# Performance work log

Measured on AMD Instinct MI355X. Metric: run time of the kernel, lower is better.

The kernel has to match this reference:

```python
import math
import jax, jax.numpy as jnp
import numpy as np

B, S, G, CMAX, T = 128, 256, 8, 6, 32
E, NH, L, Z = 64, 4, 2, 3
DFF = 4 * E


def _conv1d(x, w, b, pad):
    # x: [N, C, T], w: [O, I, K] -> [N, O, T]
    y = jax.lax.conv_general_dilated(x, w, (1,), [(pad, pad)], dimension_numbers=('NCH', 'OIH', 'NCH'))
    return y + b[None, :, None]


def _layernorm(x, g, b, eps=1e-5):
    m = jnp.mean(x, -1, keepdims=True)
    v = jnp.mean((x - m) ** 2, -1, keepdims=True)
    return (x - m) * jax.lax.rsqrt(v + eps) * g + b


def _pos_encoding(seq_len, dim):
    pos = jnp.arange(seq_len, dtype=jnp.float32)[:, None]
    div = jnp.exp(jnp.arange(0, dim, 2, dtype=jnp.float32) * (-math.log(10000.0) / dim))
    pe = jnp.zeros((seq_len, dim), dtype=jnp.float32)
    pe = pe.at[:, 0::2].set(jnp.sin(pos * div)).at[:, 1::2].set(jnp.cos(pos * div))
    return pe


def setup_inputs() -> dict:
    key = jax.random.key(0)
    ks = iter(jax.random.split(key, 48))
    def nrm(shape, s=0.05):
        return (jax.random.normal(next(ks), shape) * s).astype(jnp.float32)
    inp = {}
    inp['waveforms'] = jax.random.normal(next(ks), (B, S, CMAX, T), dtype=jnp.float32)
    inp['shank_ids'] = jax.random.randint(next(ks), (B, S), 0, G)
    lengths = jax.random.randint(next(ks), (B,), S // 2, S + 1)
    inp['mask'] = jnp.arange(S)[None, :] >= lengths[:, None]  # True = padded
    inp['conv1_w'] = nrm((G, 32, CMAX, 5), 0.1)
    inp['conv1_b'] = jnp.zeros((G, 32), jnp.float32)
    inp['conv2_w'] = nrm((G, E, 32, 3), 0.1)
    inp['conv2_b'] = jnp.zeros((G, E), jnp.float32)
    inp['shank_emb'] = nrm((G, E), 0.02)
    inp['in_proj_w'] = nrm((L, 3 * E, E))
    inp['in_proj_b'] = jnp.zeros((L, 3 * E), jnp.float32)
    inp['out_proj_w'] = nrm((L, E, E))
    inp['out_proj_b'] = jnp.zeros((L, E), jnp.float32)
    inp['ln1_g'] = jnp.ones((L, E), jnp.float32)
    inp['ln1_b'] = jnp.zeros((L, E), jnp.float32)
    inp['ff1_w'] = nrm((L, DFF, E))
    inp['ff1_b'] = jnp.zeros((L, DFF), jnp.float32)
    inp['ff2_w'] = nrm((L, E, DFF))
    inp['ff2_b'] = jnp.zeros((L, E), jnp.float32)
    inp['ln2_g'] = jnp.ones((L, E), jnp.float32)
    inp['ln2_b'] = jnp.zeros((L, E), jnp.float32)
    inp['cls_w1'] = nrm((E, E)); inp['cls_b1'] = jnp.zeros((E,), jnp.float32)
    inp['cls_w2'] = nrm((Z, E)); inp['cls_b2'] = jnp.zeros((Z,), jnp.float32)
    inp['mu_w1'] = nrm((Z, E, E)); inp['mu_b1'] = jnp.zeros((Z, E), jnp.float32)
    inp['mu_w2'] = nrm((Z, 2, E)); inp['mu_b2'] = jnp.zeros((Z, 2), jnp.float32)
    inp['ls_w1'] = nrm((Z, E, E)); inp['ls_b1'] = jnp.zeros((Z, E), jnp.float32)
    inp['ls_w2'] = nrm((Z, 2, E)); inp['ls_b2'] = jnp.zeros((Z, 2), jnp.float32)
    inp['d_w1'] = nrm((E, E)); inp['d_b1'] = jnp.zeros((E,), jnp.float32)
    inp['d_w2'] = nrm((1, E)); inp['d_b2'] = jnp.zeros((1,), jnp.float32)
    return inp


def reference(waveforms, shank_ids, mask, conv1_w, conv1_b, conv2_w, conv2_b, shank_emb,
              in_proj_w, in_proj_b, out_proj_w, out_proj_b, ln1_g, ln1_b,
              ff1_w, ff1_b, ff2_w, ff2_b, ln2_g, ln2_b,
              cls_w1, cls_b1, cls_w2, cls_b2, mu_w1, mu_b1, mu_w2, mu_b2,
              ls_w1, ls_b1, ls_w2, ls_b2, d_w1, d_b1, d_w2, d_b2):
    b, s, c, t = waveforms.shape
    e = shank_emb.shape[1]
    g = shank_emb.shape[0]
    x = waveforms.reshape(b * s, c, t)
    # per-shank conv encoders (MoE-style dispatch); loop over fixed small expert set
    embs = []
    for i in range(g):
        h1 = jax.nn.relu(_conv1d(x, conv1_w[i], conv1_b[i], 2))   # [N,32,T]
        h2 = jax.nn.relu(_conv1d(h1, conv2_w[i], conv2_b[i], 1))  # [N,E,T]
        embs.append(h2.mean(-1))                                  # AdaptiveAvgPool1d(1)
    emb_all = jnp.stack(embs, axis=1)                             # [N,G,E]
    sid = shank_ids.reshape(-1)
    emb = jnp.take_along_axis(emb_all, sid[:, None, None], axis=1)[:, 0]  # [N,E]
    active = (~mask).reshape(-1)
    emb = jnp.where(active[:, None], emb, 0.0).reshape(b, s, e)   # masked slots stay zero
    emb = emb + shank_emb[shank_ids] + _pos_encoding(s, e)[None]
    # post-norm transformer encoder, relu FFN, eval mode (dropout off)
    dh = e // NH
    key_bias = jnp.where(mask, -1e9, 0.0).astype(emb.dtype)[:, None, None, :]  # [B,1,1,S]
    h = emb
    for l in range(in_proj_w.shape[0]):
        qkv = h @ in_proj_w[l].T + in_proj_b[l]
        q, k, v = jnp.split(qkv, 3, axis=-1)
        q = q.reshape(b, s, NH, dh)
        k = k.reshape(b, s, NH, dh)
        v = v.reshape(b, s, NH, dh)
        scores = jnp.einsum('bqhd,bkhd->bhqk', q, k) / math.sqrt(dh) + key_bias
        attn = jax.nn.softmax(scores, axis=-1)
        o = jnp.einsum('bhqk,bkhd->bqhd', attn, v).reshape(b, s, e)
        o = o @ out_proj_w[l].T + out_proj_b[l]
        h = _layernorm(h + o, ln1_g[l], ln1_b[l])
        ff = jax.nn.relu(h @ ff1_w[l].T + ff1_b[l]) @ ff2_w[l].T + ff2_b[l]
        h = _layernorm(h + ff, ln2_g[l], ln2_b[l])
    am = active.reshape(b, s, 1).astype(h.dtype)
    pooled = (h * am).sum(1) / (am.sum(1) + 1e-8)                 # masked mean pool [B,E]
    cls_logits = jax.nn.relu(pooled @ cls_w1.T + cls_b1) @ cls_w2.T + cls_b2
    hz = jax.nn.relu(jnp.einsum('be,zfe->zbf', pooled, mu_w1) + mu_b1[:, None])
    mus = jnp.einsum('zbf,zof->bzo', hz, mu_w2) + mu_b2[None]     # [B,Z,2]
    hs = jax.nn.relu(jnp.einsum('be,zfe->zbf', pooled, ls_w1) + ls_b1[:, None])
    sigmas = jnp.exp(jnp.einsum('zbf,zof->bzo', hs, ls_w2) + ls_b2[None])  # [B,Z,2]
    d_pred = jax.nn.sigmoid(jax.nn.relu(pooled @ d_w1.T + d_b1) @ d_w2.T + d_b2)
    return jnp.concatenate([cls_logits, mus.reshape(b, -1), sigmas.reshape(b, -1), d_pred], axis=-1)
```

## Files before the change

kernel.cpp:

```cpp
#include <hip/hip_runtime.h>
#include <math.h>


typedef short bf16x8 __attribute__((ext_vector_type(8)));
typedef float f32x4 __attribute__((ext_vector_type(4)));

__device__ __forceinline__ unsigned short f2bf(float f) {
  unsigned u = __float_as_uint(f);
  u += 0x7fffu + ((u >> 16) & 1u);
  return (unsigned short)(u >> 16);
}

__device__ __forceinline__ float bf2f(unsigned short s) {
  return __uint_as_float(((unsigned)s) << 16);
}

__device__ __forceinline__ bf16x8 ldfrag(const unsigned short* p) {
  return *reinterpret_cast<const bf16x8*>(p);
}

__device__ __forceinline__ bool is_masked(const void* mask_, int flag, int idx) {
  return flag ? (((const unsigned char*)mask_)[idx] != 0)
              : (((const int*)mask_)[idx] != 0);
}

__global__ void detect_mask_kernel(const unsigned int* __restrict__ mw,
                                   int* __restrict__ flag, int* __restrict__ counts,
                                   int* __restrict__ lens) {
  __shared__ int sh;
  if (threadIdx.x == 0) sh = 0;
  __syncthreads();
  int bad = 0;
  for (int i = threadIdx.x; i < 8192; i += 256)
    if (mw[i] > 1u) bad = 1;
  if (bad) atomicOr(&sh, 1);
  if (threadIdx.x < 8) counts[threadIdx.x] = 0;
  if (threadIdx.x < 128) lens[threadIdx.x] = 0;
  __syncthreads();
  if (threadIdx.x == 0) *flag = sh;
}

__global__ __launch_bounds__(256) void bin_kernel(
    const int* __restrict__ sid, const void* __restrict__ mask_,
    const int* __restrict__ flagp, int* __restrict__ counts,
    int* __restrict__ lens, int* __restrict__ idxbuf) {
  __shared__ int lcnt[8];
  __shared__ int lbase[8];
  int b = blockIdx.x, tid = threadIdx.x;
  int n = b * 256 + tid;
  int flag = *flagp;
  bool act = !is_masked(mask_, flag, n);
  int g = act ? sid[n] : 0;
  if (tid < 8) lcnt[tid] = 0;
  __syncthreads();
  int pos = 0;
  if (act) pos = atomicAdd(&lcnt[g], 1);
  __syncthreads();
  if (tid < 8) lbase[tid] = atomicAdd(&counts[tid], lcnt[tid]);
  if (tid == 0)
    lens[b] = lcnt[0] + lcnt[1] + lcnt[2] + lcnt[3] +
              lcnt[4] + lcnt[5] + lcnt[6] + lcnt[7];
  __syncthreads();
  if (act) idxbuf[g * 32768 + lbase[g] + pos] = n;
}

__global__ __launch_bounds__(256) void init_emb_kernel(
    const int* __restrict__ sid, const float* __restrict__ shank_emb,
    float* __restrict__ hout) {
  int i = blockIdx.x * 256 + threadIdx.x;
  int n = i >> 6, e = i & 63, s = n & 255;
  int g = sid[n];
  float div = __expf(-(float)(e & ~1) * (9.21034037f / 64.f));
  float angle = (float)s * div;
  float pe = (e & 1) ? cosf(angle) : sinf(angle);
  hout[i] = shank_emb[g * 64 + e] + pe;
}

__global__ __launch_bounds__(256) void conv_mfma_kernel(
    const int* __restrict__ idxbuf, const int* __restrict__ counts,
    const float* __restrict__ wav,
    const float* __restrict__ w1_, const float* __restrict__ b1_,
    const float* __restrict__ w2_, const float* __restrict__ b2_,
    const float* __restrict__ shank_emb, float* __restrict__ hout) {
  __shared__ __align__(16) unsigned short w1f[5][32][8];
  __shared__ __align__(16) unsigned short w2f[3][64][40];
  __shared__ float b1s[32];
  __shared__ float b2s[64];
  __shared__ __align__(16) unsigned short xw[4][36][8];
  __shared__ __align__(16) unsigned short h1w[4][34][40];
  int g = blockIdx.x & 7, bib = blockIdx.x >> 3;
  int tid = threadIdx.x;
  int wv = tid >> 6, lane = tid & 63, quad = lane >> 4, l15 = lane & 15;
  for (int i = tid; i < 1280; i += 256) {
    int k = i >> 8, rest = i & 255, oc = rest >> 3, ic = rest & 7;
    w1f[k][oc][ic] = (ic < 6) ? f2bf(w1_[g * 960 + oc * 30 + ic * 5 + k]) : 0;
  }
  for (int i = tid; i < 7680; i += 256) {
    int k = i / 2560, rest = i % 2560, e = rest / 40, ic = rest % 40;
    w2f[k][e][ic] = (ic < 32) ? f2bf(w2_[g * 6144 + e * 96 + ic * 3 + k]) : 0;
  }
  if (tid < 32) b1s[tid] = b1_[g * 32 + tid];
  if (tid < 64) b2s[tid] = b2_[g * 64 + tid];
  {
    unsigned int* xz = (unsigned int*)&xw[wv][0][0];
    for (int i = lane; i < 144; i += 64) xz[i] = 0;
    unsigned int* hz0 = (unsigned int*)&h1w[wv][0][0];
    unsigned int* hz1 = (unsigned int*)&h1w[wv][33][0];
    if (lane < 20) hz0[lane] = 0;
    else if (lane < 40) hz1[lane - 20] = 0;
  }
  __syncthreads();
  bf16x8 zf = {0, 0, 0, 0, 0, 0, 0, 0};
  bf16x8 bf1[2], bf1k4[2], bf2[3][4];
#pragma unroll
  for (int nt = 0; nt < 2; nt++) {
    bf1[nt] = ldfrag(&w1f[quad][nt * 16 + l15][0]);
    bf1k4[nt] = (quad == 0) ? ldfrag(&w1f[4][nt * 16 + l15][0]) : zf;
  }
#pragma unroll
  for (int k = 0; k < 3; k++)
#pragma unroll
    for (int nt = 0; nt < 4; nt++)
      bf2[k][nt] = ldfrag(&w2f[k][nt * 16 + l15][quad * 8]);
  float b1v0 = b1s[l15], b1v1 = b1s[16 + l15];
  float shank = shank_emb[g * 64 + lane];
  float dive = __expf(-(float)(lane & ~1) * (9.21034037f / 64.f));
  int cnt = counts[g];
  int wvg = bib * 4 + wv;
  int ic_w = lane >> 3, t0_w = (lane & 7) * 4;
  for (int ti = wvg; ti < cnt; ti += 512) {
    int n = idxbuf[g * 32768 + ti];
    float4 v = make_float4(0.f, 0.f, 0.f, 0.f);
    if (lane < 48) v = *(const float4*)&wav[n * 192 + lane * 4];
    if (lane < 48) {
      xw[wv][t0_w + 2][ic_w] = f2bf(v.x);
      xw[wv][t0_w + 3][ic_w] = f2bf(v.y);
      xw[wv][t0_w + 4][ic_w] = f2bf(v.z);
      xw[wv][t0_w + 5][ic_w] = f2bf(v.w);
    }
    f32x4 c1[2][2];
#pragma unroll
    for (int mt = 0; mt < 2; mt++) {
      c1[mt][0] = (f32x4){b1v0, b1v0, b1v0, b1v0};
      c1[mt][1] = (f32x4){b1v1, b1v1, b1v1, b1v1};
    }
#pragma unroll
    for (int mt = 0; mt < 2; mt++) {
      bf16x8 afm = ldfrag(&xw[wv][mt * 16 + l15 + quad][0]);
      bf16x8 af4 = (quad == 0) ? ldfrag(&xw[wv][mt * 16 + l15 + 4][0]) : zf;
#pragma unroll
      for (int nt = 0; nt < 2; nt++) {
        c1[mt][nt] = __builtin_amdgcn_mfma_f32_16x16x32_bf16(afm, bf1[nt], c1[mt][nt], 0, 0, 0);
        c1[mt][nt] = __builtin_amdgcn_mfma_f32_16x16x32_bf16(af4, bf1k4[nt], c1[mt][nt], 0, 0, 0);
      }
    }
#pragma unroll
    for (int mt = 0; mt < 2; mt++)
#pragma unroll
      for (int nt = 0; nt < 2; nt++)
#pragma unroll
        for (int r = 0; r < 4; r++) {
          int t = mt * 16 + quad * 4 + r;
          h1w[wv][t + 1][nt * 16 + l15] = f2bf(fmaxf(c1[mt][nt][r], 0.f));
        }
    f32x4 c2[2][4];
#pragma unroll
    for (int mt = 0; mt < 2; mt++)
#pragma unroll
      for (int nt = 0; nt < 4; nt++) {
        float bv = b2s[nt * 16 + l15];
        c2[mt][nt] = (f32x4){bv, bv, bv, bv};
      }
#pragma unroll
    for (int k = 0; k < 3; k++)
#pragma unroll
      for (int mt = 0; mt < 2; mt++) {
        bf16x8 af = ldfrag(&h1w[wv][mt * 16 + l15 + k][quad * 8]);
#pragma unroll
        for (int nt = 0; nt < 4; nt++)
          c2[mt][nt] = __builtin_amdgcn_mfma_f32_16x16x32_bf16(af, bf2[k][nt], c2[mt][nt], 0, 0, 0);
      }
    float sums[4];
#pragma unroll
    for (int nt = 0; nt < 4; nt++) {
      float s = 0.f;
#pragma unroll
      for (int mt = 0; mt < 2; mt++)
#pragma unroll
        for (int r = 0; r < 4; r++) s += fmaxf(c2[mt][nt][r], 0.f);
      s += __shfl_xor(s, 16);
      s += __shfl_xor(s, 32);
      sums[nt] = s;
    }
    float t0 = __shfl(sums[0], l15);
    float t1 = __shfl(sums[1], l15);
    float t2 = __shfl(sums[2], l15);
    float t3 = __shfl(sums[3], l15);
    float val = (quad == 0) ? t0 : (quad == 1) ? t1 : (quad == 2) ? t2 : t3;
    float angle = (float)(n & 255) * dive;
    float pe = (lane & 1) ? cosf(angle) : sinf(angle);
    hout[(size_t)n * 64 + lane] = val * (1.f / 32.f) + shank + pe;
  }
}

__global__ __launch_bounds__(256) void gemm_qkv(
    const float* __restrict__ A, const float* __restrict__ W,
    const float* __restrict__ bias, float* __restrict__ C) {
  __shared__ __align__(16) unsigned short As[64][72];
  __shared__ __align__(16) unsigned short Bs[192][72];
  int m0 = blockIdx.x * 64;
  int tid = threadIdx.x;
  int wv = tid >> 6, lane = tid & 63, quad = lane >> 4, l15 = lane & 15;
  f32x4 acc[12];
#pragma unroll
  for (int nt = 0; nt < 12; nt++) {
    float b = bias[nt * 16 + l15];
    acc[nt] = (f32x4){b, b, b, b};
  }
  for (int i = tid; i < 1024; i += 256) {
    int r = i >> 4, c4 = (i & 15) << 2;
    float4 av = *(const float4*)&A[(size_t)(m0 + r) * 64 + c4];
    short4 t;
    t.x = (short)f2bf(av.x); t.y = (short)f2bf(av.y);
    t.z = (short)f2bf(av.z); t.w = (short)f2bf(av.w);
    *(short4*)&As[r][c4] = t;
  }
  for (int i = tid; i < 3072; i += 256) {
    int r = i >> 4, c4 = (i & 15) << 2;
    float4 wv4 = *(const float4*)&W[(size_t)r * 64 + c4];
    short4 u;
    u.x = (short)f2bf(wv4.x); u.y = (short)f2bf(wv4.y);
    u.z = (short)f2bf(wv4.z); u.w = (short)f2bf(wv4.w);
    *(short4*)&Bs[r][c4] = u;
  }
  __syncthreads();
#pragma unroll
  for (int ks = 0; ks < 64; ks += 32) {
    bf16x8 af = ldfrag(&As[wv * 16 + l15][ks + quad * 8]);
#pragma unroll
    for (int nt = 0; nt < 12; nt++) {
      bf16x8 bfr = ldfrag(&Bs[nt * 16 + l15][ks + quad * 8]);
      acc[nt] = __builtin_amdgcn_mfma_f32_16x16x32_bf16(af, bfr, acc[nt], 0, 0, 0);
    }
  }
  int mrow = m0 + wv * 16 + quad * 4;
#pragma unroll
  for (int nt = 0; nt < 12; nt++)
#pragma unroll
    for (int r = 0; r < 4; r++)
      C[(size_t)(mrow + r) * 192 + nt * 16 + l15] = acc[nt][r];
}

__global__ __launch_bounds__(256) void fused_rl_kernel(
    const float* __restrict__ obuf, float* __restrict__ H,
    const float* __restrict__ Wout, const float* __restrict__ bout,
    const float* __restrict__ ln1g, const float* __restrict__ ln1b,
    const float* __restrict__ Wff1, const float* __restrict__ bff1,
    const float* __restrict__ Wff2, const float* __restrict__ bff2,
    const float* __restrict__ ln2g, const float* __restrict__ ln2b) {
  __shared__ __align__(16) unsigned short Ao[64][72];
  __shared__ __align__(16) unsigned short Wo[64][72];
  __shared__ __align__(16) unsigned short W1s[256][72];
  __shared__ __align__(16) unsigned short W2s[64][264];
  __shared__ __align__(16) unsigned short h1b[64][72];
  __shared__ __align__(16) unsigned short ffa[64][264];
  __shared__ float h1f[64][68];
  int m0 = blockIdx.x * 64;
  int tid = threadIdx.x;
  int wv = tid >> 6, lane = tid & 63, quad = lane >> 4, l15 = lane & 15;
  for (int i = tid; i < 1024; i += 256) {
    int r = i >> 4, c4 = (i & 15) << 2;
    float4 av = *(const float4*)&obuf[(size_t)(m0 + r) * 64 + c4];
    short4 t;
    t.x = (short)f2bf(av.x); t.y = (short)f2bf(av.y);
    t.z = (short)f2bf(av.z); t.w = (short)f2bf(av.w);
    *(short4*)&Ao[r][c4] = t;
    float4 wv4 = *(const float4*)&Wout[(size_t)r * 64 + c4];
    short4 u;
    u.x = (short)f2bf(wv4.x); u.y = (short)f2bf(wv4.y);
    u.z = (short)f2bf(wv4.z); u.w = (short)f2bf(wv4.w);
    *(short4*)&Wo[r][c4] = u;
  }
  for (int i = tid; i < 4096; i += 256) {
    int r = i >> 4, c4 = (i & 15) << 2;
    float4 wv4 = *(const float4*)&Wff1[(size_t)r * 64 + c4];
    short4 u;
    u.x = (short)f2bf(wv4.x); u.y = (short)f2bf(wv4.y);
    u.z = (short)f2bf(wv4.z); u.w = (short)f2bf(wv4.w);
    *(short4*)&W1s[r][c4] = u;
  }
  for (int i = tid; i < 4096; i += 256) {
    int r = i >> 6, c4 = (i & 63) << 2;
    float4 wv4 = *(const float4*)&Wff2[(size_t)r * 256 + c4];
    short4 u;
    u.x = (short)f2bf(wv4.x); u.y = (short)f2bf(wv4.y);
    u.z = (short)f2bf(wv4.z); u.w = (short)f2bf(wv4.w);
    *(short4*)&W2s[r][c4] = u;
  }
  __syncthreads();
  int lr = wv * 16 + quad * 4;
  f32x4 acc[4];
#pragma unroll
  for (int nt = 0; nt < 4; nt++) {
    float b = bout[nt * 16 + l15];
    acc[nt] = (f32x4){b, b, b, b};
  }
#pragma unroll
  for (int ks = 0; ks < 64; ks += 32) {
    bf16x8 af = ldfrag(&Ao[wv * 16 + l15][ks + quad * 8]);
#pragma unroll
    for (int nt = 0; nt < 4; nt++) {
      bf16x8 bfr = ldfrag(&Wo[nt * 16 + l15][ks + quad * 8]);
      acc[nt] = __builtin_amdgcn_mfma_f32_16x16x32_bf16(af, bfr, acc[nt], 0, 0, 0);
    }
  }
#pragma unroll
  for (int r = 0; r < 4; r++) {
    float rv[4];
    float s = 0.f;
#pragma unroll
    for (int nt = 0; nt < 4; nt++) {
      float v = acc[nt][r] + H[(size_t)(m0 + lr + r) * 64 + nt * 16 + l15];
      rv[nt] = v; s += v;
    }
    s += __shfl_xor(s, 1); s += __shfl_xor(s, 2);
    s += __shfl_xor(s, 4); s += __shfl_xor(s, 8);
    float mean = s * (1.f / 64.f);
    float vsum = 0.f;
#pragma unroll
    for (int nt = 0; nt < 4; nt++) { rv[nt] -= mean; vsum += rv[nt] * rv[nt]; }
    vsum += __shfl_xor(vsum, 1); vsum += __shfl_xor(vsum, 2);
    vsum += __shfl_xor(vsum, 4); vsum += __shfl_xor(vsum, 8);
    float inv = rsqrtf(vsum * (1.f / 64.f) + 1e-5f);
#pragma unroll
    for (int nt = 0; nt < 4; nt++) {
      int col = nt * 16 + l15;
      float hv = rv[nt] * inv * ln1g[col] + ln1b[col];
      h1f[lr + r][col] = hv;
      h1b[lr + r][col] = f2bf(hv);
    }
  }
  f32x4 a2[16];
#pragma unroll
  for (int nt = 0; nt < 16; nt++) {
    float b = bff1[nt * 16 + l15];
    a2[nt] = (f32x4){b, b, b, b};
  }
#pragma unroll
  for (int ks = 0; ks < 64; ks += 32) {
    bf16x8 af = ldfrag(&h1b[wv * 16 + l15][ks + quad * 8]);
#pragma unroll
    for (int nt = 0; nt < 16; nt++) {
      bf16x8 bfr = ldfrag(&W1s[nt * 16 + l15][ks + quad * 8]);
      a2[nt] = __builtin_amdgcn_mfma_f32_16x16x32_bf16(af, bfr, a2[nt], 0, 0, 0);
    }
  }
#pragma unroll
  for (int nt = 0; nt < 16; nt++)
#pragma unroll
    for (int r = 0; r < 4; r++)
      ffa[lr + r][nt * 16 + l15] = f2bf(fmaxf(a2[nt][r], 0.f));
#pragma unroll
  for (int nt = 0; nt < 4; nt++) {
    float b = bff2[nt * 16 + l15];
    acc[nt] = (f32x4){b, b, b, b};
  }
#pragma unroll
  for (int ks = 0; ks < 256; ks += 32) {
    bf16x8 af = ldfrag(&ffa[wv * 16 + l15][ks + quad * 8]);
#pragma unroll
    for (int nt = 0; nt < 4; nt++) {
      bf16x8 bfr = ldfrag(&W2s[nt * 16 + l15][ks + quad * 8]);
      acc[nt] = __builtin_amdgcn_mfma_f32_16x16x32_bf16(af, bfr, acc[nt], 0, 0, 0);
    }
  }
#pragma unroll
  for (int r = 0; r < 4; r++) {
    float rv[4];
    float s = 0.f;
#pragma unroll
    for (int nt = 0; nt < 4; nt++) {
      float v = acc[nt][r] + h1f[lr + r][nt * 16 + l15];
      rv[nt] = v; s += v;
    }
    s += __shfl_xor(s, 1); s += __shfl_xor(s, 2);
    s += __shfl_xor(s, 4); s += __shfl_xor(s, 8);
    float mean = s * (1.f / 64.f);
    float vsum = 0.f;
#pragma unroll
    for (int nt = 0; nt < 4; nt++) { rv[nt] -= mean; vsum += rv[nt] * rv[nt]; }
    vsum += __shfl_xor(vsum, 1); vsum += __shfl_xor(vsum, 2);
    vsum += __shfl_xor(vsum, 4); vsum += __shfl_xor(vsum, 8);
    float inv = rsqrtf(vsum * (1.f / 64.f) + 1e-5f);
#pragma unroll
    for (int nt = 0; nt < 4; nt++) {
      int col = nt * 16 + l15;
      H[(size_t)(m0 + lr + r) * 64 + col] = rv[nt] * inv * ln2g[col] + ln2b[col];
    }
  }
}

__global__ __launch_bounds__(256) void attn_kernel(
    const float* __restrict__ qkv, const int* __restrict__ lens,
    float* __restrict__ o) {
  __shared__ __align__(16) unsigned short qs[256][24];
  __shared__ __align__(16) unsigned short kst[256][24];
  __shared__ __align__(16) unsigned short vT[16][264];
  __shared__ __align__(16) unsigned short pw[4][16][264];
  int bh = blockIdx.x;
  int b_ = bh >> 2, hd = bh & 3;
  int tid = threadIdx.x;
  int wv = tid >> 6, lane = tid & 63, quad = lane >> 4, l15 = lane & 15;
  int len = lens[b_];
  const float* base = qkv + b_ * 256 * 192 + hd * 16;
  for (int i = tid; i < 1024; i += 256) {
    int s = i >> 2, c = (i & 3) << 2;
    const float* rp = base + s * 192;
    float4 q4 = *(const float4*)(rp + c);
    float4 k4 = *(const float4*)(rp + 64 + c);
    float4 v4 = *(const float4*)(rp + 128 + c);
    short4 qp, kp;
    qp.x = (short)f2bf(q4.x * 0.25f); qp.y = (short)f2bf(q4.y * 0.25f);
    qp.z = (short)f2bf(q4.z * 0.25f); qp.w = (short)f2bf(q4.w * 0.25f);
    kp.x = (short)f2bf(k4.x); kp.y = (short)f2bf(k4.y);
    kp.z = (short)f2bf(k4.z); kp.w = (short)f2bf(k4.w);
    *(short4*)&qs[s][c] = qp;
    *(short4*)&kst[s][c] = kp;
    vT[c + 0][s] = f2bf(v4.x);
    vT[c + 1][s] = f2bf(v4.y);
    vT[c + 2][s] = f2bf(v4.z);
    vT[c + 3][s] = f2bf(v4.w);
  }
  __syncthreads();
  bf16x8 zf = {0, 0, 0, 0, 0, 0, 0, 0};
  f32x4 zero = {0.f, 0.f, 0.f, 0.f};
#pragma unroll 1
  for (int j = 0; j < 4; j++) {
    int qt = wv * 4 + j;
    bf16x8 bq = (quad < 2) ? ldfrag(&qs[qt * 16 + l15][quad * 8]) : zf;
    f32x4 s[16];
#pragma unroll
    for (int t = 0; t < 16; t++) {
      bf16x8 ak = (quad < 2) ? ldfrag(&kst[t * 16 + l15][quad * 8]) : zf;
      s[t] = __builtin_amdgcn_mfma_f32_16x16x32_bf16(ak, bq, zero, 0, 0, 0);
    }
    float mx = -1e30f;
#pragma unroll
    for (int t = 0; t < 16; t++)
#pragma unroll
      for (int r = 0; r < 4; r++) {
        int key = t * 16 + quad * 4 + r;
        float v = (key < len) ? s[t][r] : -1e30f;
        s[t][r] = v;
        mx = fmaxf(mx, v);
      }
    mx = fmaxf(mx, __shfl_xor(mx, 16));
    mx = fmaxf(mx, __shfl_xor(mx, 32));
    float sum = 0.f;
#pragma unroll
    for (int t = 0; t < 16; t++)
#pragma unroll
      for (int r = 0; r < 4; r++) {
        float p = __expf(s[t][r] - mx);
        s[t][r] = p;
        sum += p;
      }
    sum += __shfl_xor(sum, 16);
    sum += __shfl_xor(sum, 32);
#pragma unroll
    for (int t = 0; t < 16; t++) {
      short4 pp;
      pp.x = (short)f2bf(s[t][0]); pp.y = (short)f2bf(s[t][1]);
      pp.z = (short)f2bf(s[t][2]); pp.w = (short)f2bf(s[t][3]);
      *(short4*)&pw[wv][l15][t * 16 + quad * 4] = pp;
    }
    f32x4 acc = zero;
#pragma unroll
    for (int c = 0; c < 8; c++) {
      bf16x8 av = ldfrag(&vT[l15][c * 32 + quad * 8]);
      bf16x8 bp = ldfrag(&pw[wv][l15][c * 32 + quad * 8]);
      acc = __builtin_amdgcn_mfma_f32_16x16x32_bf16(av, bp, acc, 0, 0, 0);
    }
    float inv = 1.f / sum;
    float4 w;
    w.x = acc[0] * inv; w.y = acc[1] * inv;
    w.z = acc[2] * inv; w.w = acc[3] * inv;
    *(float4*)&o[(size_t)(b_ * 256 + qt * 16 + l15) * 64 + hd * 16 + quad * 4] = w;
  }
}

__global__ __launch_bounds__(256) void pool_kernel(
    const float* __restrict__ h, const int* __restrict__ lens,
    float* __restrict__ pooled) {
  __shared__ float ps[4][64];
  int b = blockIdx.x;
  int e = threadIdx.x & 63, sp = threadIdx.x >> 6;
  int len = lens[b];
  float sum = 0.f;
  int send = min(sp * 64 + 64, len);
  for (int s = sp * 64; s < send; s++) sum += h[(b * 256 + s) * 64 + e];
  ps[sp][e] = sum;
  __syncthreads();
  if (sp == 0) {
    float tot = ps[0][e] + ps[1][e] + ps[2][e] + ps[3][e];
    pooled[b * 64 + e] = tot / ((float)len + 1e-8f);
  }
}

__global__ __launch_bounds__(64) void heads_kernel(
    const float* __restrict__ pooled,
    const float* __restrict__ cls_w1, const float* __restrict__ cls_b1,
    const float* __restrict__ cls_w2, const float* __restrict__ cls_b2,
    const float* __restrict__ mu_w1, const float* __restrict__ mu_b1,
    const float* __restrict__ mu_w2, const float* __restrict__ mu_b2,
    const float* __restrict__ ls_w1, const float* __restrict__ ls_b1,
    const float* __restrict__ ls_w2, const float* __restrict__ ls_b2,
    const float* __restrict__ d_w1, const float* __restrict__ d_b1,
    const float* __restrict__ d_w2, const float* __restrict__ d_b2,
    float* __restrict__ out) {
  int b = blockIdx.x, e = threadIdx.x;
  __shared__ float p[64];
  __shared__ float t1[64];
  p[e] = pooled[b * 64 + e];
  __syncthreads();
  {
    float a = cls_b1[e];
    for (int j = 0; j < 64; j++) a += p[j] * cls_w1[e * 64 + j];
    t1[e] = fmaxf(a, 0.f);
  }
  __syncthreads();
  if (e < 3) {
    float a2 = cls_b2[e];
    for (int j = 0; j < 64; j++) a2 += t1[j] * cls_w2[e * 64 + j];
    out[b * 16 + e] = a2;
  }
  for (int z = 0; z < 3; z++) {
    __syncthreads();
    {
      float a = mu_b1[z * 64 + e];
      for (int j = 0; j < 64; j++) a += p[j] * mu_w1[(z * 64 + e) * 64 + j];
      t1[e] = fmaxf(a, 0.f);
    }
    __syncthreads();
    if (e < 2) {
      float a2 = mu_b2[z * 2 + e];
      for (int j = 0; j < 64; j++) a2 += t1[j] * mu_w2[(z * 2 + e) * 64 + j];
      out[b * 16 + 3 + z * 2 + e] = a2;
    }
    __syncthreads();
    {
      float a = ls_b1[z * 64 + e];
      for (int j = 0; j < 64; j++) a += p[j] * ls_w1[(z * 64 + e) * 64 + j];
      t1[e] = fmaxf(a, 0.f);
    }
    __syncthreads();
    if (e < 2) {
      float a2 = ls_b2[z * 2 + e];
      for (int j = 0; j < 64; j++) a2 += t1[j] * ls_w2[(z * 2 + e) * 64 + j];
      out[b * 16 + 9 + z * 2 + e] = __expf(a2);
    }
  }
  __syncthreads();
  {
    float a = d_b1[e];
    for (int j = 0; j < 64; j++) a += p[j] * d_w1[e * 64 + j];
    t1[e] = fmaxf(a, 0.f);
  }
  __syncthreads();
  if (e == 0) {
    float a2 = d_b2[0];
    for (int j = 0; j < 64; j++) a2 += t1[j] * d_w2[j];
    out[b * 16 + 15] = 1.f / (1.f + __expf(-a2));
  }
}

extern "C" void kernel_launch(void* const* d_in, const int* in_sizes, int n_in,
                              void* d_out, int out_size, void* d_ws, size_t ws_size,
                              hipStream_t stream) {
  const float* wav       = (const float*)d_in[0];
  const int*   sid       = (const int*)d_in[1];
  const void*  mask      = d_in[2];
  const float* conv1_w   = (const float*)d_in[3];
  const float* conv1_b   = (const float*)d_in[4];
  const float* conv2_w   = (const float*)d_in[5];
  const float* conv2_b   = (const float*)d_in[6];
  const float* shank_emb = (const float*)d_in[7];
  const float* in_proj_w = (const float*)d_in[8];
  const float* in_proj_b = (const float*)d_in[9];
  const float* out_proj_w= (const float*)d_in[10];
  const float* out_proj_b= (const float*)d_in[11];
  const float* ln1_g     = (const float*)d_in[12];
  const float* ln1_b     = (const float*)d_in[13];
  const float* ff1_w     = (const float*)d_in[14];
  const float* ff1_b     = (const float*)d_in[15];
  const float* ff2_w     = (const float*)d_in[16];
  const float* ff2_b     = (const float*)d_in[17];
  const float* ln2_g     = (const float*)d_in[18];
  const float* ln2_b     = (const float*)d_in[19];
  const float* cls_w1    = (const float*)d_in[20];
  const float* cls_b1    = (const float*)d_in[21];
  const float* cls_w2    = (const float*)d_in[22];
  const float* cls_b2    = (const float*)d_in[23];
  const float* mu_w1     = (const float*)d_in[24];
  const float* mu_b1     = (const float*)d_in[25];
  const float* mu_w2     = (const float*)d_in[26];
  const float* mu_b2     = (const float*)d_in[27];
  const float* ls_w1     = (const float*)d_in[28];
  const float* ls_b1     = (const float*)d_in[29];
  const float* ls_w2     = (const float*)d_in[30];
  const float* ls_b2     = (const float*)d_in[31];
  const float* d_w1      = (const float*)d_in[32];
  const float* d_b1      = (const float*)d_in[33];
  const float* d_w2      = (const float*)d_in[34];
  const float* d_b2      = (const float*)d_in[35];
  float* out = (float*)d_out;

  float* ws = (float*)d_ws;
  float* h      = ws;
  float* qkv    = ws + 2097152;
  float* obuf   = ws + 8388608;
  float* pooled = ws + 10485760;
  int*   ip     = (int*)(ws + 10493952);
  int*   flag   = ip;
  int*   counts = ip + 8;
  int*   lens   = ip + 16;
  int*   idxbuf = ip + 144;

  detect_mask_kernel<<<1, 256, 0, stream>>>((const unsigned int*)mask, flag, counts, lens);
  bin_kernel<<<128, 256, 0, stream>>>(sid, mask, flag, counts, lens, idxbuf);
  init_emb_kernel<<<8192, 256, 0, stream>>>(sid, shank_emb, h);
  conv_mfma_kernel<<<1024, 256, 0, stream>>>(idxbuf, counts, wav, conv1_w, conv1_b,
                                             conv2_w, conv2_b, shank_emb, h);
  for (int l = 0; l < 2; l++) {
    gemm_qkv<<<512, 256, 0, stream>>>(h, in_proj_w + l * 12288, in_proj_b + l * 192, qkv);
    attn_kernel<<<512, 256, 0, stream>>>(qkv, lens, obuf);
    fused_rl_kernel<<<512, 256, 0, stream>>>(
        obuf, h, out_proj_w + l * 4096, out_proj_b + l * 64,
        ln1_g + l * 64, ln1_b + l * 64,
        ff1_w + l * 16384, ff1_b + l * 256,
        ff2_w + l * 16384, ff2_b + l * 64,
        ln2_g + l * 64, ln2_b + l * 64);
  }
  pool_kernel<<<128, 256, 0, stream>>>(h, lens, pooled);
  heads_kernel<<<128, 64, 0, stream>>>(pooled, cls_w1, cls_b1, cls_w2, cls_b2,
                                       mu_w1, mu_b1, mu_w2, mu_b2,
                                       ls_w1, ls_b1, ls_w2, ls_b2,
                                       d_w1, d_b1, d_w2, d_b2, out);
}
```

Baseline: 340.8 us.

## Fuse QKV projection into attention kernel and merge pooling with heads

The separate QKV GEMM is removed. Each attention block (one per batch and head) now loads that sequence's hidden states and the 16-row Q/K/V weight slices, computes Q, K and V^T in shared memory with MFMA, and runs attention directly. This avoids writing and re-reading the full QKV tensor in global memory and saves one launch per layer, but the hidden states are reloaded four times, once per head. Pooling and the output heads are also merged into one kernel to drop a launch and the pooled buffer.

Result: faster. 321.9 us (-5.5%).

```diff
diff --git a/kernel.cpp b/kernel.cpp
--- a/kernel.cpp
+++ b/kernel.cpp
@@ -9,10 +9,6 @@
   unsigned u = __float_as_uint(f);
   u += 0x7fffu + ((u >> 16) & 1u);
   return (unsigned short)(u >> 16);
-}
-
-__device__ __forceinline__ float bf2f(unsigned short s) {
-  return __uint_as_float(((unsigned)s) << 16);
 }
 
 __device__ __forceinline__ bf16x8 ldfrag(const unsigned short* p) {
@@ -90,7 +86,7 @@
   __shared__ __align__(16) unsigned short h1w[4][34][40];
   int g = blockIdx.x & 7, bib = blockIdx.x >> 3;
   int tid = threadIdx.x;
-  int wv = tid >> 6, lane = tid & 63, quad = lane >> 4, l15 = lane & 15;
+  int wvx = tid >> 6, lane = tid & 63, quad = lane >> 4, l15 = lane & 15;
   for (int i = tid; i < 1280; i += 256) {
     int k = i >> 8, rest = i & 255, oc = rest >> 3, ic = rest & 7;
     w1f[k][oc][ic] = (ic < 6) ? f2bf(w1_[g * 960 + oc * 30 + ic * 5 + k]) : 0;
@@ -102,10 +98,10 @@
   if (tid < 32) b1s[tid] = b1_[g * 32 + tid];
   if (tid < 64) b2s[tid] = b2_[g * 64 + tid];
   {
-    unsigned int* xz = (unsigned int*)&xw[wv][0][0];
+    unsigned int* xz = (unsigned int*)&xw[wvx][0][0];
     for (int i = lane; i < 144; i += 64) xz[i] = 0;
-    unsigned int* hz0 = (unsigned int*)&h1w[wv][0][0];
-    unsigned int* hz1 = (unsigned int*)&h1w[wv][33][0];
+    unsigned int* hz0 = (unsigned int*)&h1w[wvx][0][0];
+    unsigned int* hz1 = (unsigned int*)&h1w[wvx][33][0];
     if (lane < 20) hz0[lane] = 0;
     else if (lane < 40) hz1[lane - 20] = 0;
   }
@@ -126,17 +122,17 @@
   float shank = shank_emb[g * 64 + lane];
   float dive = __expf(-(float)(lane & ~1) * (9.21034037f / 64.f));
   int cnt = counts[g];
-  int wvg = bib * 4 + wv;
+  int wvg = bib * 4 + wvx;
   int ic_w = lane >> 3, t0_w = (lane & 7) * 4;
   for (int ti = wvg; ti < cnt; ti += 512) {
     int n = idxbuf[g * 32768 + ti];
     float4 v = make_float4(0.f, 0.f, 0.f, 0.f);
     if (lane < 48) v = *(const float4*)&wav[n * 192 + lane * 4];
     if (lane < 48) {
-      xw[wv][t0_w + 2][ic_w] = f2bf(v.x);
-      xw[wv][t0_w + 3][ic_w] = f2bf(v.y);
-      xw[wv][t0_w + 4][ic_w] = f2bf(v.z);
-      xw[wv][t0_w + 5][ic_w] = f2bf(v.w);
+      xw[wvx][t0_w + 2][ic_w] = f2bf(v.x);
+      xw[wvx][t0_w + 3][ic_w] = f2bf(v.y);
+      xw[wvx][t0_w + 4][ic_w] = f2bf(v.z);
+      xw[wvx][t0_w + 5][ic_w] = f2bf(v.w);
     }
     f32x4 c1[2][2];
 #pragma unroll
@@ -146,8 +142,8 @@
     }
 #pragma unroll
     for (int mt = 0; mt < 2; mt++) {
-      bf16x8 afm = ldfrag(&xw[wv][mt * 16 + l15 + quad][0]);
-      bf16x8 af4 = (quad == 0) ? ldfrag(&xw[wv][mt * 16 + l15 + 4][0]) : zf;
+      bf16x8 afm = ldfrag(&xw[wvx][mt * 16 + l15 + quad][0]);
+      bf16x8 af4 = (quad == 0) ? ldfrag(&xw[wvx][mt * 16 + l15 + 4][0]) : zf;
 #pragma unroll
       for (int nt = 0; nt < 2; nt++) {
         c1[mt][nt] = __builtin_amdgcn_mfma_f32_16x16x32_bf16(afm, bf1[nt], c1[mt][nt], 0, 0, 0);
@@ -161,7 +157,7 @@
 #pragma unroll
         for (int r = 0; r < 4; r++) {
           int t = mt * 16 + quad * 4 + r;
-          h1w[wv][t + 1][nt * 16 + l15] = f2bf(fmaxf(c1[mt][nt][r], 0.f));
+          h1w[wvx][t + 1][nt * 16 + l15] = f2bf(fmaxf(c1[mt][nt][r], 0.f));
         }
     f32x4 c2[2][4];
 #pragma unroll
@@ -175,7 +171,7 @@
     for (int k = 0; k < 3; k++)
 #pragma unroll
       for (int mt = 0; mt < 2; mt++) {
-        bf16x8 af = ldfrag(&h1w[wv][mt * 16 + l15 + k][quad * 8]);
+        bf16x8 af = ldfrag(&h1w[wvx][mt * 16 + l15 + k][quad * 8]);
 #pragma unroll
         for (int nt = 0; nt < 4; nt++)
           c2[mt][nt] = __builtin_amdgcn_mfma_f32_16x16x32_bf16(af, bf2[k][nt], c2[mt][nt], 0, 0, 0);
@@ -203,52 +199,129 @@
   }
 }
 
-__global__ __launch_bounds__(256) void gemm_qkv(
-    const float* __restrict__ A, const float* __restrict__ W,
-    const float* __restrict__ bias, float* __restrict__ C) {
-  __shared__ __align__(16) unsigned short As[64][72];
-  __shared__ __align__(16) unsigned short Bs[192][72];
-  int m0 = blockIdx.x * 64;
+__global__ __launch_bounds__(256) void attn_fused_kernel(
+    const float* __restrict__ H, const float* __restrict__ Wqkv,
+    const float* __restrict__ bqkv, const int* __restrict__ lens,
+    float* __restrict__ o) {
+  __shared__ __align__(16) unsigned short un[18432];
+  __shared__ __align__(16) unsigned short wqs[16][72];
+  __shared__ __align__(16) unsigned short wks[16][72];
+  __shared__ __align__(16) unsigned short wvs[16][72];
+  __shared__ __align__(16) unsigned short qs[256][24];
+  __shared__ __align__(16) unsigned short kst[256][24];
+  __shared__ __align__(16) unsigned short vT[16][264];
+  __shared__ float bqs[16], bks[16], bvs[16];
+  unsigned short (*hs)[72] = (unsigned short(*)[72])un;
+  unsigned short (*pw)[16][264] = (unsigned short(*)[16][264])un;
+  int bh = blockIdx.x;
+  int b_ = bh >> 2, hd = bh & 3;
   int tid = threadIdx.x;
-  int wv = tid >> 6, lane = tid & 63, quad = lane >> 4, l15 = lane & 15;
-  f32x4 acc[12];
-#pragma unroll
-  for (int nt = 0; nt < 12; nt++) {
-    float b = bias[nt * 16 + l15];
-    acc[nt] = (f32x4){b, b, b, b};
-  }
-  for (int i = tid; i < 1024; i += 256) {
+  int wvx = tid >> 6, lane = tid & 63, quad = lane >> 4, l15 = lane & 15;
+  int len = lens[b_];
+  const float* hb = H + (size_t)b_ * 256 * 64;
+  for (int i = tid; i < 4096; i += 256) {
     int r = i >> 4, c4 = (i & 15) << 2;
-    float4 av = *(const float4*)&A[(size_t)(m0 + r) * 64 + c4];
+    float4 v = *(const float4*)&hb[r * 64 + c4];
     short4 t;
-    t.x = (short)f2bf(av.x); t.y = (short)f2bf(av.y);
-    t.z = (short)f2bf(av.z); t.w = (short)f2bf(av.w);
-    *(short4*)&As[r][c4] = t;
-  }
-  for (int i = tid; i < 3072; i += 256) {
+    t.x = (short)f2bf(v.x); t.y = (short)f2bf(v.y);
+    t.z = (short)f2bf(v.z); t.w = (short)f2bf(v.w);
+    *(short4*)&hs[r][c4] = t;
+  }
+  for (int i = tid; i < 768; i += 256) {
     int r = i >> 4, c4 = (i & 15) << 2;
-    float4 wv4 = *(const float4*)&W[(size_t)r * 64 + c4];
-    short4 u;
-    u.x = (short)f2bf(wv4.x); u.y = (short)f2bf(wv4.y);
-    u.z = (short)f2bf(wv4.z); u.w = (short)f2bf(wv4.w);
-    *(short4*)&Bs[r][c4] = u;
-  }
-  __syncthreads();
-#pragma unroll
-  for (int ks = 0; ks < 64; ks += 32) {
-    bf16x8 af = ldfrag(&As[wv * 16 + l15][ks + quad * 8]);
-#pragma unroll
-    for (int nt = 0; nt < 12; nt++) {
-      bf16x8 bfr = ldfrag(&Bs[nt * 16 + l15][ks + quad * 8]);
-      acc[nt] = __builtin_amdgcn_mfma_f32_16x16x32_bf16(af, bfr, acc[nt], 0, 0, 0);
-    }
-  }
-  int mrow = m0 + wv * 16 + quad * 4;
-#pragma unroll
-  for (int nt = 0; nt < 12; nt++)
-#pragma unroll
-    for (int r = 0; r < 4; r++)
-      C[(size_t)(mrow + r) * 192 + nt * 16 + l15] = acc[nt][r];
+    int which = r >> 4, rr = r & 15;
+    float4 v = *(const float4*)&Wqkv[(size_t)(which * 64 + hd * 16 + rr) * 64 + c4];
+    float sc = (which == 0) ? 0.25f : 1.f;
+    short4 t;
+    t.x = (short)f2bf(v.x * sc); t.y = (short)f2bf(v.y * sc);
+    t.z = (short)f2bf(v.z * sc); t.w = (short)f2bf(v.w * sc);
+    unsigned short (*dst)[72] = (which == 0) ? wqs : (which == 1) ? wks : wvs;
+    *(short4*)&dst[rr][c4] = t;
+  }
+  if (tid < 16) {
+    bqs[tid] = 0.25f * bqkv[hd * 16 + tid];
+    bks[tid] = bqkv[64 + hd * 16 + tid];
+    bvs[tid] = bqkv[128 + hd * 16 + tid];
+  }
+  __syncthreads();
+#pragma unroll
+  for (int t4 = 0; t4 < 4; t4++) {
+    int tile = wvx * 4 + t4;
+    float bq = bqs[l15], bk = bks[l15];
+    f32x4 aq = (f32x4){bq, bq, bq, bq};
+    f32x4 ak = (f32x4){bk, bk, bk, bk};
+    f32x4 av = (f32x4){bvs[quad * 4 + 0], bvs[quad * 4 + 1],
+                       bvs[quad * 4 + 2], bvs[quad * 4 + 3]};
+#pragma unroll
+    for (int ks = 0; ks < 64; ks += 32) {
+      bf16x8 af = ldfrag(&hs[tile * 16 + l15][ks + quad * 8]);
+      aq = __builtin_amdgcn_mfma_f32_16x16x32_bf16(af, ldfrag(&wqs[l15][ks + quad * 8]), aq, 0, 0, 0);
+      ak = __builtin_amdgcn_mfma_f32_16x16x32_bf16(af, ldfrag(&wks[l15][ks + quad * 8]), ak, 0, 0, 0);
+      av = __builtin_amdgcn_mfma_f32_16x16x32_bf16(ldfrag(&wvs[l15][ks + quad * 8]), af, av, 0, 0, 0);
+    }
+#pragma unroll
+    for (int r = 0; r < 4; r++) {
+      qs[tile * 16 + quad * 4 + r][l15] = f2bf(aq[r]);
+      kst[tile * 16 + quad * 4 + r][l15] = f2bf(ak[r]);
+      vT[quad * 4 + r][tile * 16 + l15] = f2bf(av[r]);
+    }
+  }
+  __syncthreads();
+  bf16x8 zf = {0, 0, 0, 0, 0, 0, 0, 0};
+  f32x4 zero = {0.f, 0.f, 0.f, 0.f};
+#pragma unroll 1
+  for (int j = 0; j < 4; j++) {
+    int qt = wvx * 4 + j;
+    bf16x8 bq = (quad < 2) ? ldfrag(&qs[qt * 16 + l15][quad * 8]) : zf;
+    f32x4 s[16];
+#pragma unroll
+    for (int t = 0; t < 16; t++) {
+      bf16x8 ak = (quad < 2) ? ldfrag(&kst[t * 16 + l15][quad * 8]) : zf;
+      s[t] = __builtin_amdgcn_mfma_f32_16x16x32_bf16(ak, bq, zero, 0, 0, 0);
+    }
+    float mx = -1e30f;
+#pragma unroll
+    for (int t = 0; t < 16; t++)
+#pragma unroll
+      for (int r = 0; r < 4; r++) {
+        int key = t * 16 + quad * 4 + r;
+        float v = (key < len) ? s[t][r] : -1e30f;
+        s[t][r] = v;
+        mx = fmaxf(mx, v);
+      }
+    mx = fmaxf(mx, __shfl_xor(mx, 16));
+    mx = fmaxf(mx, __shfl_xor(mx, 32));
+    float sum = 0.f;
+#pragma unroll
+    for (int t = 0; t < 16; t++)
+#pragma unroll
+      for (int r = 0; r < 4; r++) {
+        float p = __expf(s[t][r] - mx);
+        s[t][r] = p;
+        sum += p;
+      }
+    sum += __shfl_xor(sum, 16);
+    sum += __shfl_xor(sum, 32);
+#pragma unroll
+    for (int t = 0; t < 16; t++) {
+      short4 pp;
+      pp.x = (short)f2bf(s[t][0]); pp.y = (short)f2bf(s[t][1]);
+      pp.z = (short)f2bf(s[t][2]); pp.w = (short)f2bf(s[t][3]);
+      *(short4*)&pw[wvx][l15][t * 16 + quad * 4] = pp;
+    }
+    f32x4 acc = zero;
+#pragma unroll
+    for (int c = 0; c < 8; c++) {
+      bf16x8 avv = ldfrag(&vT[l15][c * 32 + quad * 8]);
+      bf16x8 bp = ldfrag(&pw[wvx][l15][c * 32 + quad * 8]);
+      acc = __builtin_amdgcn_mfma_f32_16x16x32_bf16(avv, bp, acc, 0, 0, 0);
+    }
+    float inv = 1.f / sum;
+    float4 w;
+    w.x = acc[0] * inv; w.y = acc[1] * inv;
+    w.z = acc[2] * inv; w.w = acc[3] * inv;
+    *(float4*)&o[(size_t)(b_ * 256 + qt * 16 + l15) * 64 + hd * 16 + quad * 4] = w;
+  }
 }
 
 __global__ __launch_bounds__(256) void fused_rl_kernel(
@@ -267,7 +340,7 @@
   __shared__ float h1f[64][68];
   int m0 = blockIdx.x * 64;
   int tid = threadIdx.x;
-  int wv = tid >> 6, lane = tid & 63, quad = lane >> 4, l15 = lane & 15;
+  int wvx = tid >> 6, lane = tid & 63, quad = lane >> 4, l15 = lane & 15;
   for (int i = tid; i < 1024; i += 256) {
     int r = i >> 4, c4 = (i & 15) << 2;
     float4 av = *(const float4*)&obuf[(size_t)(m0 + r) * 64 + c4];
@@ -298,7 +371,7 @@
     *(short4*)&W2s[r][c4] = u;
   }
   __syncthreads();
-  int lr = wv * 16 + quad * 4;
+  int lr = wvx * 16 + quad * 4;
   f32x4 acc[4];
 #pragma unroll
   for (int nt = 0; nt < 4; nt++) {
@@ -307,7 +380,7 @@
   }
 #pragma unroll
   for (int ks = 0; ks < 64; ks += 32) {
-    bf16x8 af = ldfrag(&Ao[wv * 16 + l15][ks + quad * 8]);
+    bf16x8 af = ldfrag(&Ao[wvx * 16 + l15][ks + quad * 8]);
 #pragma unroll
     for (int nt = 0; nt < 4; nt++) {
       bf16x8 bfr = ldfrag(&Wo[nt * 16 + l15][ks + quad * 8]);
@@ -348,7 +421,7 @@
   }
 #pragma unroll
   for (int ks = 0; ks < 64; ks += 32) {
-    bf16x8 af = ldfrag(&h1b[wv * 16 + l15][ks + quad * 8]);
+    bf16x8 af = ldfrag(&h1b[wvx * 16 + l15][ks + quad * 8]);
 #pragma unroll
     for (int nt = 0; nt < 16; nt++) {
       bf16x8 bfr = ldfrag(&W1s[nt * 16 + l15][ks + quad * 8]);
@@ -367,7 +440,7 @@
   }
 #pragma unroll
   for (int ks = 0; ks < 256; ks += 32) {
-    bf16x8 af = ldfrag(&ffa[wv * 16 + l15][ks + quad * 8]);
+    bf16x8 af = ldfrag(&ffa[wvx * 16 + l15][ks + quad * 8]);
 #pragma unroll
     for (int nt = 0; nt < 4; nt++) {
       bf16x8 bfr = ldfrag(&W2s[nt * 16 + l15][ks + quad * 8]);
@@ -400,115 +473,8 @@
   }
 }
 
-__global__ __launch_bounds__(256) void attn_kernel(
-    const float* __restrict__ qkv, const int* __restrict__ lens,
-    float* __restrict__ o) {
-  __shared__ __align__(16) unsigned short qs[256][24];
-  __shared__ __align__(16) unsigned short kst[256][24];
-  __shared__ __align__(16) unsigned short vT[16][264];
-  __shared__ __align__(16) unsigned short pw[4][16][264];
-  int bh = blockIdx.x;
-  int b_ = bh >> 2, hd = bh & 3;
-  int tid = threadIdx.x;
-  int wv = tid >> 6, lane = tid & 63, quad = lane >> 4, l15 = lane & 15;
-  int len = lens[b_];
-  const float* base = qkv + b_ * 256 * 192 + hd * 16;
-  for (int i = tid; i < 1024; i += 256) {
-    int s = i >> 2, c = (i & 3) << 2;
-    const float* rp = base + s * 192;
-    float4 q4 = *(const float4*)(rp + c);
-    float4 k4 = *(const float4*)(rp + 64 + c);
-    float4 v4 = *(const float4*)(rp + 128 + c);
-    short4 qp, kp;
-    qp.x = (short)f2bf(q4.x * 0.25f); qp.y = (short)f2bf(q4.y * 0.25f);
-    qp.z = (short)f2bf(q4.z * 0.25f); qp.w = (short)f2bf(q4.w * 0.25f);
-    kp.x = (short)f2bf(k4.x); kp.y = (short)f2bf(k4.y);
-    kp.z = (short)f2bf(k4.z); kp.w = (short)f2bf(k4.w);
-    *(short4*)&qs[s][c] = qp;
-    *(short4*)&kst[s][c] = kp;
-    vT[c + 0][s] = f2bf(v4.x);
-    vT[c + 1][s] = f2bf(v4.y);
-    vT[c + 2][s] = f2bf(v4.z);
-    vT[c + 3][s] = f2bf(v4.w);
-  }
-  __syncthreads();
-  bf16x8 zf = {0, 0, 0, 0, 0, 0, 0, 0};
-  f32x4 zero = {0.f, 0.f, 0.f, 0.f};
-#pragma unroll 1
-  for (int j = 0; j < 4; j++) {
-    int qt = wv * 4 + j;
-    bf16x8 bq = (quad < 2) ? ldfrag(&qs[qt * 16 + l15][quad * 8]) : zf;
-    f32x4 s[16];
-#pragma unroll
-    for (int t = 0; t < 16; t++) {
-      bf16x8 ak = (quad < 2) ? ldfrag(&kst[t * 16 + l15][quad * 8]) : zf;
-      s[t] = __builtin_amdgcn_mfma_f32_16x16x32_bf16(ak, bq, zero, 0, 0, 0);
-    }
-    float mx = -1e30f;
-#pragma unroll
-    for (int t = 0; t < 16; t++)
-#pragma unroll
-      for (int r = 0; r < 4; r++) {
-        int key = t * 16 + quad * 4 + r;
-        float v = (key < len) ? s[t][r] : -1e30f;
-        s[t][r] = v;
-        mx = fmaxf(mx, v);
-      }
-    mx = fmaxf(mx, __shfl_xor(mx, 16));
-    mx = fmaxf(mx, __shfl_xor(mx, 32));
-    float sum = 0.f;
-#pragma unroll
-    for (int t = 0; t < 16; t++)
-#pragma unroll
-      for (int r = 0; r < 4; r++) {
-        float p = __expf(s[t][r] - mx);
-        s[t][r] = p;
-        sum += p;
-      }
-    sum += __shfl_xor(sum, 16);
-    sum += __shfl_xor(sum, 32);
-#pragma unroll
-    for (int t = 0; t < 16; t++) {
-      short4 pp;
-      pp.x = (short)f2bf(s[t][0]); pp.y = (short)f2bf(s[t][1]);
-      pp.z = (short)f2bf(s[t][2]); pp.w = (short)f2bf(s[t][3]);
-      *(short4*)&pw[wv][l15][t * 16 + quad * 4] = pp;
-    }
-    f32x4 acc = zero;
-#pragma unroll
-    for (int c = 0; c < 8; c++) {
-      bf16x8 av = ldfrag(&vT[l15][c * 32 + quad * 8]);
-      bf16x8 bp = ldfrag(&pw[wv][l15][c * 32 + quad * 8]);
-      acc = __builtin_amdgcn_mfma_f32_16x16x32_bf16(av, bp, acc, 0, 0, 0);
-    }
-    float inv = 1.f / sum;
-    float4 w;
-    w.x = acc[0] * inv; w.y = acc[1] * inv;
-    w.z = acc[2] * inv; w.w = acc[3] * inv;
-    *(float4*)&o[(size_t)(b_ * 256 + qt * 16 + l15) * 64 + hd * 16 + quad * 4] = w;
-  }
-}
-
-__global__ __launch_bounds__(256) void pool_kernel(
+__global__ __launch_bounds__(256) void pool_heads_kernel(
     const float* __restrict__ h, const int* __restrict__ lens,
-    float* __restrict__ pooled) {
-  __shared__ float ps[4][64];
-  int b = blockIdx.x;
-  int e = threadIdx.x & 63, sp = threadIdx.x >> 6;
-  int len = lens[b];
-  float sum = 0.f;
-  int send = min(sp * 64 + 64, len);
-  for (int s = sp * 64; s < send; s++) sum += h[(b * 256 + s) * 64 + e];
-  ps[sp][e] = sum;
-  __syncthreads();
-  if (sp == 0) {
-    float tot = ps[0][e] + ps[1][e] + ps[2][e] + ps[3][e];
-    pooled[b * 64 + e] = tot / ((float)len + 1e-8f);
-  }
-}
-
-__global__ __launch_bounds__(64) void heads_kernel(
-    const float* __restrict__ pooled,
     const float* __restrict__ cls_w1, const float* __restrict__ cls_b1,
     const float* __restrict__ cls_w2, const float* __restrict__ cls_b2,
     const float* __restrict__ mu_w1, const float* __restrict__ mu_b1,
@@ -518,56 +484,67 @@
     const float* __restrict__ d_w1, const float* __restrict__ d_b1,
     const float* __restrict__ d_w2, const float* __restrict__ d_b2,
     float* __restrict__ out) {
-  int b = blockIdx.x, e = threadIdx.x;
+  __shared__ float ps[4][64];
   __shared__ float p[64];
   __shared__ float t1[64];
-  p[e] = pooled[b * 64 + e];
-  __syncthreads();
+  int b = blockIdx.x, tid = threadIdx.x;
+  int e = tid & 63, sp = tid >> 6;
+  int len = lens[b];
   {
-    float a = cls_b1[e];
-    for (int j = 0; j < 64; j++) a += p[j] * cls_w1[e * 64 + j];
-    t1[e] = fmaxf(a, 0.f);
-  }
-  __syncthreads();
-  if (e < 3) {
-    float a2 = cls_b2[e];
-    for (int j = 0; j < 64; j++) a2 += t1[j] * cls_w2[e * 64 + j];
-    out[b * 16 + e] = a2;
+    float sum = 0.f;
+    int send = min(sp * 64 + 64, len);
+    for (int s = sp * 64; s < send; s++) sum += h[(size_t)(b * 256 + s) * 64 + e];
+    ps[sp][e] = sum;
+  }
+  __syncthreads();
+  if (sp == 0)
+    p[e] = (ps[0][e] + ps[1][e] + ps[2][e] + ps[3][e]) / ((float)len + 1e-8f);
+  __syncthreads();
+  if (tid < 64) {
+    float a = cls_b1[tid];
+    for (int j = 0; j < 64; j++) a += p[j] * cls_w1[tid * 64 + j];
+    t1[tid] = fmaxf(a, 0.f);
+  }
+  __syncthreads();
+  if (tid < 3) {
+    float a2 = cls_b2[tid];
+    for (int j = 0; j < 64; j++) a2 += t1[j] * cls_w2[tid * 64 + j];
+    out[b * 16 + tid] = a2;
   }
   for (int z = 0; z < 3; z++) {
     __syncthreads();
-    {
-      float a = mu_b1[z * 64 + e];
-      for (int j = 0; j < 64; j++) a += p[j] * mu_w1[(z * 64 + e) * 64 + j];
-      t1[e] = fmaxf(a, 0.f);
+    if (tid < 64) {
+      float a = mu_b1[z * 64 + tid];
+      for (int j = 0; j < 64; j++) a += p[j] * mu_w1[(z * 64 + tid) * 64 + j];
+      t1[tid] = fmaxf(a, 0.f);
     }
     __syncthreads();
-    if (e < 2) {
-      float a2 = mu_b2[z * 2 + e];
-      for (int j = 0; j < 64; j++) a2 += t1[j] * mu_w2[(z * 2 + e) * 64 + j];
-      out[b * 16 + 3 + z * 2 + e] = a2;
+    if (tid < 2) {
+      float a2 = mu_b2[z * 2 + tid];
+      for (int j = 0; j < 64; j++) a2 += t1[j] * mu_w2[(z * 2 + tid) * 64 + j];
+      out[b * 16 + 3 + z * 2 + tid] = a2;
     }
     __syncthreads();
-    {
-      float a = ls_b1[z * 64 + e];
-      for (int j = 0; j < 64; j++) a += p[j] * ls_w1[(z * 64 + e) * 64 + j];
-      t1[e] = fmaxf(a, 0.f);
+    if (tid < 64) {
+      float a = ls_b1[z * 64 + tid];
+      for (int j = 0; j < 64; j++) a += p[j] * ls_w1[(z * 64 + tid) * 64 + j];
+      t1[tid] = fmaxf(a, 0.f);
     }
     __syncthreads();
-    if (e < 2) {
-      float a2 = ls_b2[z * 2 + e];
-      for (int j = 0; j < 64; j++) a2 += t1[j] * ls_w2[(z * 2 + e) * 64 + j];
-      out[b * 16 + 9 + z * 2 + e] = __expf(a2);
-    }
-  }
-  __syncthreads();
-  {
-    float a = d_b1[e];
-    for (int j = 0; j < 64; j++) a += p[j] * d_w1[e * 64 + j];
-    t1[e] = fmaxf(a, 0.f);
-  }
-  __syncthreads();
-  if (e == 0) {
+    if (tid < 2) {
+      float a2 = ls_b2[z * 2 + tid];
+      for (int j = 0; j < 64; j++) a2 += t1[j] * ls_w2[(z * 2 + tid) * 64 + j];
+      out[b * 16 + 9 + z * 2 + tid] = __expf(a2);
+    }
+  }
+  __syncthreads();
+  if (tid < 64) {
+    float a = d_b1[tid];
+    for (int j = 0; j < 64; j++) a += p[j] * d_w1[tid * 64 + j];
+    t1[tid] = fmaxf(a, 0.f);
+  }
+  __syncthreads();
+  if (tid == 0) {
     float a2 = d_b2[0];
     for (int j = 0; j < 64; j++) a2 += t1[j] * d_w2[j];
     out[b * 16 + 15] = 1.f / (1.f + __expf(-a2));
@@ -617,9 +594,7 @@
 
   float* ws = (float*)d_ws;
   float* h      = ws;
-  float* qkv    = ws + 2097152;
-  float* obuf   = ws + 8388608;
-  float* pooled = ws + 10485760;
+  float* obuf   = ws + 2097152;
   int*   ip     = (int*)(ws + 10493952);
   int*   flag   = ip;
   int*   counts = ip + 8;
@@ -632,8 +607,8 @@
   conv_mfma_kernel<<<1024, 256, 0, stream>>>(idxbuf, counts, wav, conv1_w, conv1_b,
                                              conv2_w, conv2_b, shank_emb, h);
   for (int l = 0; l < 2; l++) {
-    gemm_qkv<<<512, 256, 0, stream>>>(h, in_proj_w + l * 12288, in_proj_b + l * 192, qkv);
-    attn_kernel<<<512, 256, 0, stream>>>(qkv, lens, obuf);
+    attn_fused_kernel<<<512, 256, 0, stream>>>(h, in_proj_w + l * 12288,
+                                               in_proj_b + l * 192, lens, obuf);
     fused_rl_kernel<<<512, 256, 0, stream>>>(
         obuf, h, out_proj_w + l * 4096, out_proj_b + l * 64,
         ln1_g + l * 64, ln1_b + l * 64,
@@ -641,9 +616,8 @@
         ff2_w + l * 16384, ff2_b + l * 64,
         ln2_g + l * 64, ln2_b + l * 64);
   }
-  pool_kernel<<<128, 256, 0, stream>>>(h, lens, pooled);
-  heads_kernel<<<128, 64, 0, stream>>>(pooled, cls_w1, cls_b1, cls_w2, cls_b2,
-                                       mu_w1, mu_b1, mu_w2, mu_b2,
-                                       ls_w1, ls_b1, ls_w2, ls_b2,
-                                       d_w1, d_b1, d_w2, d_b2, out);
-}
+  pool_heads_kernel<<<128, 256, 0, stream>>>(h, lens, cls_w1, cls_b1, cls_w2, cls_b2,
+                                             mu_w1, mu_b1, mu_w2, mu_b2,
+                                             ls_w1, ls_b1, ls_w2, ls_b2,
+                                             d_w1, d_b1, d_w2, d_b2, out);
+}
```
